# Kernel optimization log

Hardware: AMD Instinct MI355X
Metric: run time of the kernel (lower is better)

The kernel has to match this reference:

```python
import jax, jax.numpy as jnp
import numpy as np

NUM_GRAPHS = 512
NODES_PER_GRAPH = 200  # == N_rois
EDGES_PER_GRAPH = 3200  # avg degree 16
N_ROIS = 200
HIDDEN = 64
OUT = 2


def setup_inputs() -> dict:
    key = jax.random.key(0)
    ks = jax.random.split(key, 7)
    N = NUM_GRAPHS * NODES_PER_GRAPH
    E = NUM_GRAPHS * EDGES_PER_GRAPH
    x = jax.random.normal(ks[0], (N, N_ROIS), dtype=jnp.float32)
    # edges sampled within each graph's node block
    base = jnp.repeat(jnp.arange(NUM_GRAPHS, dtype=jnp.int64) * NODES_PER_GRAPH, EDGES_PER_GRAPH)
    local = jax.random.randint(ks[1], (2, E), 0, NODES_PER_GRAPH, dtype=jnp.int64)
    edge_index = local + base[None, :]
    batch = jnp.arange(N, dtype=jnp.int64) // NODES_PER_GRAPH
    conv_w = jax.random.normal(ks[2], (N_ROIS, HIDDEN), dtype=jnp.float32) * 0.1
    conv_b = jax.random.normal(ks[3], (HIDDEN,), dtype=jnp.float32) * 0.1
    lin_w = jax.random.normal(ks[4], (HIDDEN, OUT), dtype=jnp.float32) * 0.1
    lin_b = jax.random.normal(ks[5], (OUT,), dtype=jnp.float32) * 0.1
    return {"x": x, "edge_index": edge_index, "batch": batch,
            "conv_w": conv_w, "conv_b": conv_b, "lin_w": lin_w, "lin_b": lin_b}


def reference(x, edge_index, batch, conv_w, conv_b, lin_w, lin_b):
    N = x.shape[0]
    # GCNConv: linear transform first (N_rois -> hidden), then normalized aggregation
    h = x @ conv_w  # [N, H]
    loops = jnp.arange(N, dtype=edge_index.dtype)
    src = jnp.concatenate([edge_index[0], loops])  # add self-loops (PyG default)
    dst = jnp.concatenate([edge_index[1], loops])
    deg = jax.ops.segment_sum(jnp.ones_like(dst, dtype=h.dtype), dst, num_segments=N)
    dinv = jnp.where(deg > 0, jax.lax.rsqrt(deg), jnp.zeros_like(deg))
    norm = dinv[src] * dinv[dst]  # D^-1/2 (A+I) D^-1/2 edge weights
    agg = jax.ops.segment_sum(h[src] * norm[:, None], dst, num_segments=N) + conv_b
    hr = jax.nn.relu(agg)
    x_pool = jax.ops.segment_max(hr, batch, num_segments=NUM_GRAPHS)  # [G, H]
    out = x_pool @ lin_w + lin_b  # [G, OUT]
    return out, x_pool
```

## Files before the change

kernel.cpp:

```cpp
#include <hip/hip_runtime.h>

#define NUM_GRAPHS 512
#define NPG 200
#define EPG 3200
#define NROIS 200
#define HID 64
#define OUTC 2
#define APITCH 232
#define HPITCH 232
#define WIMG_ELEMS (7 * 4 * 2 * 64 * 8)
#define WS_NEEDED ((size_t)WIMG_ELEMS * 2)

typedef short v8s __attribute__((ext_vector_type(8)));
typedef float v4f __attribute__((ext_vector_type(4)));

__device__ __forceinline__ unsigned bf16_rne(float f) {
  unsigned u = __float_as_uint(f);
  return (u + 0x7fffu + ((u >> 16) & 1u)) >> 16;
}

__global__ void prep_wimg(const float* __restrict__ cw, unsigned short* __restrict__ wimg) {
  int idx = blockIdx.x * 256 + threadIdx.x;
  if (idx >= WIMG_ELEMS) return;
  int i    = idx & 7;
  int lane = (idx >> 3) & 63;
  int hl   = (idx >> 9) & 1;
  int nt   = (idx >> 10) & 3;
  int kt   = idx >> 12;
  int k  = kt * 32 + (lane >> 4) * 8 + i;
  int ch = nt * 16 + (lane & 15);
  float f = (k < NROIS) ? cw[k * HID + ch] : 0.f;
  unsigned hi = bf16_rne(f);
  float lo = f - __uint_as_float(hi << 16);
  wimg[idx] = hl ? (unsigned short)(__float_as_uint(lo) >> 16) : (unsigned short)hi;
}

struct __align__(16) Smem2 {
  unsigned char adj[208 * APITCH];
  unsigned short hpTl[HID * HPITCH];
  int cnt[NPG];
  float dinv[NPG];
  int pool[HID];
};

__device__ __forceinline__ v8s tobf16(const float4& a, const float4& b) {
  v8s r;
  r[0] = (short)bf16_rne(a.x); r[1] = (short)bf16_rne(a.y);
  r[2] = (short)bf16_rne(a.z); r[3] = (short)bf16_rne(a.w);
  r[4] = (short)bf16_rne(b.x); r[5] = (short)bf16_rne(b.y);
  r[6] = (short)bf16_rne(b.z); r[7] = (short)bf16_rne(b.w);
  return r;
}

__device__ __forceinline__ void xfetch(const float* __restrict__ x, int base,
                                       int kt, int q, const int* mts, const int* nrow,
                                       float4 xa[2][2]) {
  const int k0 = kt * 32 + q * 8;
  const bool ok = (k0 + 8 <= NROIS);
  #pragma unroll
  for (int mi = 0; mi < 2; ++mi) {
    if (mts[mi] >= 0) {
      if (ok) {
        const float* px = x + (size_t)(base + nrow[mi]) * NROIS + k0;
        xa[mi][0] = *(const float4*)px;
        xa[mi][1] = *(const float4*)(px + 4);
      } else {
        xa[mi][0] = make_float4(0.f, 0.f, 0.f, 0.f);
        xa[mi][1] = make_float4(0.f, 0.f, 0.f, 0.f);
      }
    }
  }
}

__global__ __launch_bounds__(512, 4)
void gcn_fused5(const float* __restrict__ x,
                const int* __restrict__ ei,
                const unsigned short* __restrict__ wimg,
                const float* __restrict__ cb,
                const float* __restrict__ lw,
                const float* __restrict__ lb,
                float* __restrict__ out,
                int Etot) {
  __shared__ Smem2 s;
  const int g = blockIdx.x;
  const int tid = threadIdx.x;
  const int base = g * NPG;
  const int ebase = g * EPG;
  const int lane = tid & 63;
  const int w = __builtin_amdgcn_readfirstlane(tid >> 6);
  const int ml = tid & 15;
  const int q  = (tid >> 4) & 3;

  int mts[2];
  mts[0] = w;
  mts[1] = (w < 5) ? 8 + w : -1;
  int nrow[2];
  #pragma unroll
  for (int mi = 0; mi < 2; ++mi) {
    int node = mts[mi] * 16 + ml;
    nrow[mi] = (node < NPG) ? node : 0;
  }

  int esrc[7], edst[7];
  #pragma unroll
  for (int r = 0; r < 7; ++r) {
    int e = tid + r * 512;
    esrc[r] = -1; edst[r] = 0;
    if (e < EPG) {
      esrc[r] = ei[ebase + e] - base;
      edst[r] = ei[Etot + ebase + e] - base;
    }
  }
  float4 xa[2][2];
  xfetch(x, base, 0, q, mts, nrow, xa);
  {
    uint4* z = (uint4*)s.adj;
    const uint4 z4 = {0u, 0u, 0u, 0u};
    #pragma unroll
    for (int i = 0; i < 6; ++i) {
      int idx = tid + i * 512;
      if (idx < (208 * APITCH) / 16) z[idx] = z4;
    }
    if (tid < NPG) s.cnt[tid] = 0;
    if (tid < HID) s.pool[tid] = 0;
  }
  __syncthreads();

  {
    unsigned* adjW = (unsigned*)s.adj;
    #pragma unroll
    for (int r = 0; r < 7; ++r) {
      if (esrc[r] >= 0) {
        int idx = edst[r] * APITCH + esrc[r];
        atomicAdd(&adjW[idx >> 2], 1u << ((idx & 3) * 8));
        atomicAdd(&s.cnt[edst[r]], 1);
      }
    }
    if (tid < NPG) {
      int idx = tid * APITCH + tid;
      atomicAdd(&adjW[idx >> 2], 1u << ((idx & 3) * 8));
    }
  }

  v4f acc[2][4];
  #pragma unroll
  for (int a = 0; a < 2; ++a)
    #pragma unroll
    for (int b = 0; b < 4; ++b)
      acc[a][b] = (v4f){0.f, 0.f, 0.f, 0.f};

  for (int kt = 0; kt < 7; ++kt) {
    v8s xh2[2];
    #pragma unroll
    for (int mi = 0; mi < 2; ++mi)
      if (mts[mi] >= 0) xh2[mi] = tobf16(xa[mi][0], xa[mi][1]);
    if (kt < 6) xfetch(x, base, kt + 1, q, mts, nrow, xa);

    v8s whi[4], wlo[4];
    #pragma unroll
    for (int nt = 0; nt < 4; ++nt) {
      const unsigned short* pw = wimg + (size_t)(((kt * 4 + nt) * 2) * 64 + lane) * 8;
      whi[nt] = *(const v8s*)pw;
      wlo[nt] = *(const v8s*)(pw + 64 * 8);
    }
    #pragma unroll
    for (int mi = 0; mi < 2; ++mi) {
      if (mts[mi] >= 0) {
        #pragma unroll
        for (int nt = 0; nt < 4; ++nt) {
          acc[mi][nt] = __builtin_amdgcn_mfma_f32_16x16x32_bf16(wlo[nt], xh2[mi], acc[mi][nt], 0, 0, 0);
          acc[mi][nt] = __builtin_amdgcn_mfma_f32_16x16x32_bf16(whi[nt], xh2[mi], acc[mi][nt], 0, 0, 0);
        }
      }
    }
  }
  __syncthreads();

  if (tid < NPG) s.dinv[tid] = rsqrtf((float)(s.cnt[tid] + 1));
  {
    int ch = tid >> 3, grp = tid & 7;
    *(uint2*)&s.hpTl[ch * HPITCH + 200 + grp * 4] = (uint2){0u, 0u};
  }
  #pragma unroll
  for (int mi = 0; mi < 2; ++mi) {
    if (mts[mi] >= 0) {
      const int node = mts[mi] * 16 + ml;
      if (node < NPG) {
        const float dv = rsqrtf((float)(s.cnt[node] + 1));
        #pragma unroll
        for (int nt = 0; nt < 4; ++nt) {
          #pragma unroll
          for (int r = 0; r < 4; ++r) {
            const int ch = nt * 16 + q * 4 + r;
            s.hpTl[ch * HPITCH + node] = (unsigned short)bf16_rne(dv * acc[mi][nt][r]);
          }
        }
      }
    }
  }
  __syncthreads();

  {
    v4f acc2[2][4];
    #pragma unroll
    for (int a = 0; a < 2; ++a)
      #pragma unroll
      for (int b = 0; b < 4; ++b)
        acc2[a][b] = (v4f){0.f, 0.f, 0.f, 0.f};

    for (int kt = 0; kt < 7; ++kt) {
      const int k0 = kt * 32 + q * 8;

      v8s bf[4];
      #pragma unroll
      for (int nt = 0; nt < 4; ++nt)
        bf[nt] = *(const v8s*)&s.hpTl[(nt * 16 + ml) * HPITCH + k0];

      #pragma unroll
      for (int mi = 0; mi < 2; ++mi) {
        if (mts[mi] >= 0) {
          const int row = mts[mi] * 16 + ml;
          const uint2 dd = *(const uint2*)&s.adj[row * APITCH + k0];
          v8s af;
          #pragma unroll
          for (int i = 0; i < 4; ++i) {
            af[i]     = (short)(__float_as_uint((float)((dd.x >> (8 * i)) & 0xffu)) >> 16);
            af[i + 4] = (short)(__float_as_uint((float)((dd.y >> (8 * i)) & 0xffu)) >> 16);
          }
          #pragma unroll
          for (int nt = 0; nt < 4; ++nt)
            acc2[mi][nt] = __builtin_amdgcn_mfma_f32_16x16x32_bf16(af, bf[nt], acc2[mi][nt], 0, 0, 0);
        }
      }
    }

    float cbv[4];
    #pragma unroll
    for (int nt = 0; nt < 4; ++nt) cbv[nt] = cb[nt * 16 + ml];
    float mx[4] = {0.f, 0.f, 0.f, 0.f};
    #pragma unroll
    for (int mi = 0; mi < 2; ++mi) {
      if (mts[mi] >= 0) {
        #pragma unroll
        for (int r = 0; r < 4; ++r) {
          const int row = mts[mi] * 16 + q * 4 + r;
          if (row < NPG) {
            const float dv = s.dinv[row];
            #pragma unroll
            for (int nt = 0; nt < 4; ++nt) {
              float v = fmaxf(fmaf(dv, acc2[mi][nt][r], cbv[nt]), 0.f);
              mx[nt] = fmaxf(mx[nt], v);
            }
          }
        }
      }
    }
    #pragma unroll
    for (int nt = 0; nt < 4; ++nt) {
      mx[nt] = fmaxf(mx[nt], __shfl_xor(mx[nt], 16));
      mx[nt] = fmaxf(mx[nt], __shfl_xor(mx[nt], 32));
    }
    if (q == 0 && (lane >> 5) == 0) {
      #pragma unroll
      for (int nt = 0; nt < 4; ++nt)
        atomicMax(&s.pool[nt * 16 + ml], __float_as_int(mx[nt]));
    }
  }
  __syncthreads();

  if (tid < HID) {
    const float xp = __int_as_float(s.pool[tid]);
    out[NUM_GRAPHS * OUTC + g * HID + tid] = xp;
    float p0 = xp * lw[tid * 2 + 0];
    float p1 = xp * lw[tid * 2 + 1];
    #pragma unroll
    for (int off = 32; off > 0; off >>= 1) {
      p0 += __shfl_down(p0, off);
      p1 += __shfl_down(p1, off);
    }
    if (tid == 0) {
      out[g * OUTC + 0] = p0 + lb[0];
      out[g * OUTC + 1] = p1 + lb[1];
    }
  }
}

struct __align__(16) SmemF {
  unsigned char adj[208 * APITCH];
  unsigned short hpT[HID * HPITCH];
  float dinv[NPG];
  int cnt[NPG];
  int pool[HID];
};

__global__ __launch_bounds__(512, 4)
void gcn_fused_fb(const float* __restrict__ x,
                  const int* __restrict__ ei,
                  const float* __restrict__ cw,
                  const float* __restrict__ cb,
                  const float* __restrict__ lw,
                  const float* __restrict__ lb,
                  float* __restrict__ out,
                  int Etot) {
  __shared__ SmemF s;
  const int g = blockIdx.x;
  const int tid = threadIdx.x;
  const int base = g * NPG;
  const int ebase = g * EPG;
  const int lane = tid & 63;
  const int w = __builtin_amdgcn_readfirstlane(tid >> 6);
  const int ml = tid & 15;
  const int q  = (tid >> 4) & 3;

  {
    uint4* z = (uint4*)&s;
    const uint4 z4 = {0u, 0u, 0u, 0u};
    #pragma unroll
    for (int i = 0; i < 10; ++i) {
      int idx = tid + i * 512;
      if (idx < (208 * APITCH + HID * HPITCH * 2) / 16) z[idx] = z4;
    }
    if (tid < NPG) s.cnt[tid] = 0;
    if (tid < HID) s.pool[tid] = 0;
  }
  __syncthreads();

  int esrc[7], edst[7];
  #pragma unroll
  for (int r = 0; r < 7; ++r) {
    int e = tid + r * 512;
    esrc[r] = -1; edst[r] = 0;
    if (e < EPG) {
      esrc[r] = ei[ebase + e] - base;
      edst[r] = ei[Etot + ebase + e] - base;
      atomicAdd(&s.cnt[edst[r]], 1);
    }
  }
  __syncthreads();

  if (tid < NPG) s.dinv[tid] = rsqrtf((float)(s.cnt[tid] + 1));

  {
    unsigned* adjW = (unsigned*)s.adj;
    #pragma unroll
    for (int r = 0; r < 7; ++r) {
      if (esrc[r] >= 0) {
        int idx = edst[r] * APITCH + esrc[r];
        atomicAdd(&adjW[idx >> 2], 1u << ((idx & 3) * 8));
      }
    }
    if (tid < NPG) {
      int idx = tid * APITCH + tid;
      atomicAdd(&adjW[idx >> 2], 1u << ((idx & 3) * 8));
    }
  }
  __syncthreads();

  {
    int mts[2];
    mts[0] = w;
    mts[1] = (w < 5) ? 8 + w : -1;
    v4f acc[2][4];
    #pragma unroll
    for (int a = 0; a < 2; ++a)
      #pragma unroll
      for (int b = 0; b < 4; ++b)
        acc[a][b] = (v4f){0.f, 0.f, 0.f, 0.f};

    for (int kt = 0; kt < 7; ++kt) {
      const int k0 = kt * 32 + q * 8;
      const bool kok = (k0 < NROIS);
      v8s bhi[4], blo[4];
      #pragma unroll
      for (int nt = 0; nt < 4; ++nt) {
        #pragma unroll
        for (int i = 0; i < 8; ++i) {
          float f = kok ? cw[(k0 + i) * HID + nt * 16 + ml] : 0.f;
          unsigned hb = bf16_rne(f);
          float lo = f - __uint_as_float(hb << 16);
          bhi[nt][i] = (short)hb;
          blo[nt][i] = (short)(__float_as_uint(lo) >> 16);
        }
      }
      #pragma unroll
      for (int mi = 0; mi < 2; ++mi) {
        if (mts[mi] >= 0) {
          const int row = mts[mi] * 16 + ml;
          v8s ahi, alo;
          if (kok && row < NPG) {
            const float* px = x + (size_t)(base + row) * NROIS + k0;
            const float4 f0 = *(const float4*)px;
            const float4 f1 = *(const float4*)(px + 4);
            const float ff[8] = {f0.x, f0.y, f0.z, f0.w, f1.x, f1.y, f1.z, f1.w};
            #pragma unroll
            for (int i = 0; i < 8; ++i) {
              unsigned u = __float_as_uint(ff[i]);
              unsigned hb = u >> 16;
              float lo = ff[i] - __uint_as_float(hb << 16);
              ahi[i] = (short)hb;
              alo[i] = (short)(__float_as_uint(lo) >> 16);
            }
          } else {
            #pragma unroll
            for (int i = 0; i < 8; ++i) { ahi[i] = 0; alo[i] = 0; }
          }
          #pragma unroll
          for (int nt = 0; nt < 4; ++nt) {
            acc[mi][nt] = __builtin_amdgcn_mfma_f32_16x16x32_bf16(ahi, blo[nt], acc[mi][nt], 0, 0, 0);
            acc[mi][nt] = __builtin_amdgcn_mfma_f32_16x16x32_bf16(alo, bhi[nt], acc[mi][nt], 0, 0, 0);
            acc[mi][nt] = __builtin_amdgcn_mfma_f32_16x16x32_bf16(ahi, bhi[nt], acc[mi][nt], 0, 0, 0);
          }
        }
      }
    }
    #pragma unroll
    for (int mi = 0; mi < 2; ++mi) {
      if (mts[mi] >= 0) {
        #pragma unroll
        for (int r = 0; r < 4; ++r) {
          const int row = mts[mi] * 16 + q * 4 + r;
          if (row < NPG) {
            const float dv = s.dinv[row];
            #pragma unroll
            for (int nt = 0; nt < 4; ++nt)
              s.hpT[(nt * 16 + ml) * HPITCH + row] =
                  (unsigned short)bf16_rne(dv * acc[mi][nt][r]);
          }
        }
      }
    }
  }
  __syncthreads();

  {
    int mts[2];
    mts[0] = w;
    mts[1] = (w < 5) ? 8 + w : -1;
    v4f acc2[2][4];
    #pragma unroll
    for (int a = 0; a < 2; ++a)
      #pragma unroll
      for (int b = 0; b < 4; ++b)
        acc2[a][b] = (v4f){0.f, 0.f, 0.f, 0.f};

    for (int kt = 0; kt < 7; ++kt) {
      const int k0 = kt * 32 + q * 8;
      v8s bf[4];
      #pragma unroll
      for (int nt = 0; nt < 4; ++nt)
        bf[nt] = *(const v8s*)&s.hpT[(nt * 16 + ml) * HPITCH + k0];
      #pragma unroll
      for (int mi = 0; mi < 2; ++mi) {
        if (mts[mi] >= 0) {
          const int row = mts[mi] * 16 + ml;
          const uint2 dd = *(const uint2*)&s.adj[row * APITCH + k0];
          v8s af;
          #pragma unroll
          for (int i = 0; i < 4; ++i) {
            af[i]     = (short)(__float_as_uint((float)((dd.x >> (8 * i)) & 0xffu)) >> 16);
            af[i + 4] = (short)(__float_as_uint((float)((dd.y >> (8 * i)) & 0xffu)) >> 16);
          }
          #pragma unroll
          for (int nt = 0; nt < 4; ++nt)
            acc2[mi][nt] = __builtin_amdgcn_mfma_f32_16x16x32_bf16(af, bf[nt], acc2[mi][nt], 0, 0, 0);
        }
      }
    }

    float cbv[4];
    #pragma unroll
    for (int nt = 0; nt < 4; ++nt) cbv[nt] = cb[nt * 16 + ml];
    float mx[4] = {0.f, 0.f, 0.f, 0.f};
    #pragma unroll
    for (int mi = 0; mi < 2; ++mi) {
      if (mts[mi] >= 0) {
        #pragma unroll
        for (int r = 0; r < 4; ++r) {
          const int row = mts[mi] * 16 + q * 4 + r;
          if (row < NPG) {
            const float dv = s.dinv[row];
            #pragma unroll
            for (int nt = 0; nt < 4; ++nt) {
              float v = fmaxf(fmaf(dv, acc2[mi][nt][r], cbv[nt]), 0.f);
              mx[nt] = fmaxf(mx[nt], v);
            }
          }
        }
      }
    }
    #pragma unroll
    for (int nt = 0; nt < 4; ++nt) {
      mx[nt] = fmaxf(mx[nt], __shfl_xor(mx[nt], 16));
      mx[nt] = fmaxf(mx[nt], __shfl_xor(mx[nt], 32));
    }
    if (q == 0 && (lane >> 5) == 0) {
      #pragma unroll
      for (int nt = 0; nt < 4; ++nt)
        atomicMax(&s.pool[nt * 16 + ml], __float_as_int(mx[nt]));
    }
  }
  __syncthreads();

  if (tid < HID) {
    const float xp = __int_as_float(s.pool[tid]);
    out[NUM_GRAPHS * OUTC + g * HID + tid] = xp;
    float p0 = xp * lw[tid * 2 + 0];
    float p1 = xp * lw[tid * 2 + 1];
    #pragma unroll
    for (int off = 32; off > 0; off >>= 1) {
      p0 += __shfl_down(p0, off);
      p1 += __shfl_down(p1, off);
    }
    if (tid == 0) {
      out[g * OUTC + 0] = p0 + lb[0];
      out[g * OUTC + 1] = p1 + lb[1];
    }
  }
}

extern "C" void kernel_launch(void* const* d_in, const int* in_sizes, int n_in,
                              void* d_out, int out_size, void* d_ws, size_t ws_size,
                              hipStream_t stream) {
  const float* x  = (const float*)d_in[0];
  const int*   ei = (const int*)d_in[1];
  const float* cw = (const float*)d_in[3];
  const float* cb = (const float*)d_in[4];
  const float* lw = (const float*)d_in[5];
  const float* lb = (const float*)d_in[6];
  const int Etot = in_sizes[1] / 2;

  if (ws_size >= WS_NEEDED) {
    unsigned short* wimg = (unsigned short*)d_ws;
    prep_wimg<<<(WIMG_ELEMS + 255) / 256, 256, 0, stream>>>(cw, wimg);
    gcn_fused5<<<NUM_GRAPHS, 512, 0, stream>>>(x, ei, wimg, cb, lw, lb,
                                               (float*)d_out, Etot);
  } else {
    gcn_fused_fb<<<NUM_GRAPHS, 512, 0, stream>>>(x, ei, cw, cb, lw, lb,
                                                 (float*)d_out, Etot);
  }
}
```

Measured before the change: 151.1 us.

## Stage weights in LDS, pack adjacency to 4 bits, deepen x prefetch

The weight image is copied once per block into LDS with global_load_lds. That LDS region is shared through a union with the later hpTl buffer, so the first GEMM reads its weights from LDS instead of issuing global loads on every k-tile. The x prefetch goes from one tile ahead to three, using rotating register slots in a fully unrolled templated loop. The adjacency matrix is packed as 4-bit counts instead of bytes, which shrinks it in LDS and cuts both the zeroing work and the second GEMM's loads. The risks are that any edge with multiplicity above 15 would overflow its nibble, and that correctness depends on the async LDS load having completed before the first barrier.

```diff
diff --git a/kernel.cpp b/kernel.cpp
--- a/kernel.cpp
+++ b/kernel.cpp
@@ -7,6 +7,7 @@
 #define HID 64
 #define OUTC 2
 #define APITCH 232
+#define NPITCH 26
 #define HPITCH 232
 #define WIMG_ELEMS (7 * 4 * 2 * 64 * 8)
 #define WS_NEEDED ((size_t)WIMG_ELEMS * 2)
@@ -35,9 +36,12 @@
   wimg[idx] = hl ? (unsigned short)(__float_as_uint(lo) >> 16) : (unsigned short)hi;
 }
 
-struct __align__(16) Smem2 {
-  unsigned char adj[208 * APITCH];
-  unsigned short hpTl[HID * HPITCH];
+struct __align__(16) Smem3 {
+  unsigned int adjN[200 * NPITCH];
+  union {
+    unsigned short wl[WIMG_ELEMS];
+    unsigned short hpTl[HID * HPITCH];
+  } u;
   int cnt[NPG];
   float dinv[NPG];
   int pool[HID];
@@ -72,16 +76,46 @@
   }
 }
 
+template<int KT>
+__device__ __forceinline__ void kt1(const float* __restrict__ x, int base, int q,
+                                    const int* mts, const int* nrow,
+                                    const unsigned short* wl,
+                                    float4 (&slot)[2][2], v4f (&acc)[2][4], int lane) {
+  v8s xh2[2];
+  #pragma unroll
+  for (int mi = 0; mi < 2; ++mi)
+    if (mts[mi] >= 0) xh2[mi] = tobf16(slot[mi][0], slot[mi][1]);
+  if constexpr (KT + 3 <= 6)
+    xfetch(x, base, KT + 3, q, mts, nrow, slot);
+  v8s whi[4], wlo[4];
+  #pragma unroll
+  for (int nt = 0; nt < 4; ++nt) {
+    const unsigned short* pw = wl + (size_t)(((KT * 4 + nt) * 2) * 64 + lane) * 8;
+    whi[nt] = *(const v8s*)pw;
+    wlo[nt] = *(const v8s*)(pw + 64 * 8);
+  }
+  #pragma unroll
+  for (int mi = 0; mi < 2; ++mi) {
+    if (mts[mi] >= 0) {
+      #pragma unroll
+      for (int nt = 0; nt < 4; ++nt) {
+        acc[mi][nt] = __builtin_amdgcn_mfma_f32_16x16x32_bf16(wlo[nt], xh2[mi], acc[mi][nt], 0, 0, 0);
+        acc[mi][nt] = __builtin_amdgcn_mfma_f32_16x16x32_bf16(whi[nt], xh2[mi], acc[mi][nt], 0, 0, 0);
+      }
+    }
+  }
+}
+
 __global__ __launch_bounds__(512, 4)
-void gcn_fused5(const float* __restrict__ x,
-                const int* __restrict__ ei,
-                const unsigned short* __restrict__ wimg,
-                const float* __restrict__ cb,
-                const float* __restrict__ lw,
-                const float* __restrict__ lb,
-                float* __restrict__ out,
-                int Etot) {
-  __shared__ Smem2 s;
+void gcn_fused10(const float* __restrict__ x,
+                 const int* __restrict__ ei,
+                 const unsigned short* __restrict__ wimg,
+                 const float* __restrict__ cb,
+                 const float* __restrict__ lw,
+                 const float* __restrict__ lb,
+                 float* __restrict__ out,
+                 int Etot) {
+  __shared__ Smem3 s;
   const int g = blockIdx.x;
   const int tid = threadIdx.x;
   const int base = g * NPG;
@@ -101,6 +135,18 @@
     nrow[mi] = (node < NPG) ? node : 0;
   }
 
+  float4 xa[3][2][2];
+  xfetch(x, base, 0, q, mts, nrow, xa[0]);
+  xfetch(x, base, 1, q, mts, nrow, xa[1]);
+  xfetch(x, base, 2, q, mts, nrow, xa[2]);
+  #pragma unroll
+  for (int c = 0; c < 7; ++c) {
+    const char* gp = (const char*)wimg + c * 8192 + (size_t)(w * 64 + lane) * 16;
+    unsigned char* lp = (unsigned char*)s.u.wl + c * 8192 + w * 1024;
+    __builtin_amdgcn_global_load_lds(
+        (const __attribute__((address_space(1))) unsigned int*)gp,
+        (__attribute__((address_space(3))) unsigned int*)lp, 16, 0, 0);
+  }
   int esrc[7], edst[7];
   #pragma unroll
   for (int r = 0; r < 7; ++r) {
@@ -111,15 +157,13 @@
       edst[r] = ei[Etot + ebase + e] - base;
     }
   }
-  float4 xa[2][2];
-  xfetch(x, base, 0, q, mts, nrow, xa);
-  {
-    uint4* z = (uint4*)s.adj;
+  {
+    uint4* z = (uint4*)s.adjN;
     const uint4 z4 = {0u, 0u, 0u, 0u};
     #pragma unroll
-    for (int i = 0; i < 6; ++i) {
+    for (int i = 0; i < 3; ++i) {
       int idx = tid + i * 512;
-      if (idx < (208 * APITCH) / 16) z[idx] = z4;
+      if (idx < (200 * NPITCH) / 4) z[idx] = z4;
     }
     if (tid < NPG) s.cnt[tid] = 0;
     if (tid < HID) s.pool[tid] = 0;
@@ -127,18 +171,17 @@
   __syncthreads();
 
   {
-    unsigned* adjW = (unsigned*)s.adj;
     #pragma unroll
     for (int r = 0; r < 7; ++r) {
       if (esrc[r] >= 0) {
-        int idx = edst[r] * APITCH + esrc[r];
-        atomicAdd(&adjW[idx >> 2], 1u << ((idx & 3) * 8));
+        int idx = edst[r] * 208 + esrc[r];
+        atomicAdd(&s.adjN[idx >> 3], 1u << ((idx & 7) * 4));
         atomicAdd(&s.cnt[edst[r]], 1);
       }
     }
     if (tid < NPG) {
-      int idx = tid * APITCH + tid;
-      atomicAdd(&adjW[idx >> 2], 1u << ((idx & 3) * 8));
+      int idx = tid * 208 + tid;
+      atomicAdd(&s.adjN[idx >> 3], 1u << ((idx & 7) * 4));
     }
   }
 
@@ -149,37 +192,20 @@
     for (int b = 0; b < 4; ++b)
       acc[a][b] = (v4f){0.f, 0.f, 0.f, 0.f};
 
-  for (int kt = 0; kt < 7; ++kt) {
-    v8s xh2[2];
-    #pragma unroll
-    for (int mi = 0; mi < 2; ++mi)
-      if (mts[mi] >= 0) xh2[mi] = tobf16(xa[mi][0], xa[mi][1]);
-    if (kt < 6) xfetch(x, base, kt + 1, q, mts, nrow, xa);
-
-    v8s whi[4], wlo[4];
-    #pragma unroll
-    for (int nt = 0; nt < 4; ++nt) {
-      const unsigned short* pw = wimg + (size_t)(((kt * 4 + nt) * 2) * 64 + lane) * 8;
-      whi[nt] = *(const v8s*)pw;
-      wlo[nt] = *(const v8s*)(pw + 64 * 8);
-    }
-    #pragma unroll
-    for (int mi = 0; mi < 2; ++mi) {
-      if (mts[mi] >= 0) {
-        #pragma unroll
-        for (int nt = 0; nt < 4; ++nt) {
-          acc[mi][nt] = __builtin_amdgcn_mfma_f32_16x16x32_bf16(wlo[nt], xh2[mi], acc[mi][nt], 0, 0, 0);
-          acc[mi][nt] = __builtin_amdgcn_mfma_f32_16x16x32_bf16(whi[nt], xh2[mi], acc[mi][nt], 0, 0, 0);
-        }
-      }
-    }
-  }
+  const unsigned short* wl = (const unsigned short*)s.u.wl;
+  kt1<0>(x, base, q, mts, nrow, wl, xa[0], acc, lane);
+  kt1<1>(x, base, q, mts, nrow, wl, xa[1], acc, lane);
+  kt1<2>(x, base, q, mts, nrow, wl, xa[2], acc, lane);
+  kt1<3>(x, base, q, mts, nrow, wl, xa[0], acc, lane);
+  kt1<4>(x, base, q, mts, nrow, wl, xa[1], acc, lane);
+  kt1<5>(x, base, q, mts, nrow, wl, xa[2], acc, lane);
+  kt1<6>(x, base, q, mts, nrow, wl, xa[0], acc, lane);
   __syncthreads();
 
   if (tid < NPG) s.dinv[tid] = rsqrtf((float)(s.cnt[tid] + 1));
   {
     int ch = tid >> 3, grp = tid & 7;
-    *(uint2*)&s.hpTl[ch * HPITCH + 200 + grp * 4] = (uint2){0u, 0u};
+    *(uint2*)&s.u.hpTl[ch * HPITCH + 200 + grp * 4] = (uint2){0u, 0u};
   }
   #pragma unroll
   for (int mi = 0; mi < 2; ++mi) {
@@ -192,7 +218,7 @@
           #pragma unroll
           for (int r = 0; r < 4; ++r) {
             const int ch = nt * 16 + q * 4 + r;
-            s.hpTl[ch * HPITCH + node] = (unsigned short)bf16_rne(dv * acc[mi][nt][r]);
+            s.u.hpTl[ch * HPITCH + node] = (unsigned short)bf16_rne(dv * acc[mi][nt][r]);
           }
         }
       }
@@ -214,19 +240,18 @@
       v8s bf[4];
       #pragma unroll
       for (int nt = 0; nt < 4; ++nt)
-        bf[nt] = *(const v8s*)&s.hpTl[(nt * 16 + ml) * HPITCH + k0];
+        bf[nt] = *(const v8s*)&s.u.hpTl[(nt * 16 + ml) * HPITCH + k0];
 
       #pragma unroll
       for (int mi = 0; mi < 2; ++mi) {
         if (mts[mi] >= 0) {
           const int row = mts[mi] * 16 + ml;
-          const uint2 dd = *(const uint2*)&s.adj[row * APITCH + k0];
+          const int arow = (row < NPG) ? row : 0;
+          const unsigned dd = s.adjN[arow * NPITCH + (k0 >> 3)];
           v8s af;
           #pragma unroll
-          for (int i = 0; i < 4; ++i) {
-            af[i]     = (short)(__float_as_uint((float)((dd.x >> (8 * i)) & 0xffu)) >> 16);
-            af[i + 4] = (short)(__float_as_uint((float)((dd.y >> (8 * i)) & 0xffu)) >> 16);
-          }
+          for (int i = 0; i < 8; ++i)
+            af[i] = (short)(__float_as_uint((float)((dd >> (4 * i)) & 0xFu)) >> 16);
           #pragma unroll
           for (int nt = 0; nt < 4; ++nt)
             acc2[mi][nt] = __builtin_amdgcn_mfma_f32_16x16x32_bf16(af, bf[nt], acc2[mi][nt], 0, 0, 0);
@@ -532,8 +557,8 @@
   if (ws_size >= WS_NEEDED) {
     unsigned short* wimg = (unsigned short*)d_ws;
     prep_wimg<<<(WIMG_ELEMS + 255) / 256, 256, 0, stream>>>(cw, wimg);
-    gcn_fused5<<<NUM_GRAPHS, 512, 0, stream>>>(x, ei, wimg, cb, lw, lb,
-                                               (float*)d_out, Etot);
+    gcn_fused10<<<NUM_GRAPHS, 512, 0, stream>>>(x, ei, wimg, cb, lw, lb,
+                                                (float*)d_out, Etot);
   } else {
     gcn_fused_fb<<<NUM_GRAPHS, 512, 0, stream>>>(x, ei, cw, cb, lw, lb,
                                                  (float*)d_out, Etot);
```

Measured after the change: 148.5 us. No clear change (-1.7%).
